# Kernel optimization log

Hardware: AMD Instinct MI355X
Metric: run time of the kernel (lower is better)

## Reference

```python
import jax, jax.numpy as jnp
import numpy as np

B, T, D = 2, 4096, 512
H = 8
HD = D // H  # 64


def setup_inputs() -> dict:
    key = jax.random.key(0)
    k1, k2, k3 = jax.random.split(key, 3)
    x = jax.random.normal(k1, (B, T, D), dtype=jnp.float32)
    w_qkv = jax.random.normal(k2, (3 * D, D), dtype=jnp.float32) * (1.0 / np.sqrt(D))
    w_out = jax.random.normal(k3, (D, D), dtype=jnp.float32) * (1.0 / np.sqrt(D))
    return {"x": x, "w_qkv": w_qkv, "w_out": w_out}


def reference(x, w_qkv, w_out):
    b, t, d = x.shape
    qkv = x @ w_qkv.T                      # [B,T,3D]
    q, k, v = jnp.split(qkv, 3, axis=-1)
    # b t (h d) -> b h t d
    def split_heads(a):
        return a.reshape(b, t, H, HD).transpose(0, 2, 1, 3)
    q, k, v = split_heads(q), split_heads(k), split_heads(v)
    scale = 1.0 / np.sqrt(HD).astype(np.float32)
    scores = jnp.einsum('bhqd,bhkd->bhqk', q, k) * scale  # [B,H,T,T]
    causal = jnp.tril(jnp.ones((t, t), dtype=bool))        # keep lower triangle
    scores = jnp.where(causal[None, None], scores, -jnp.inf)
    attn = jax.nn.softmax(scores, axis=-1)
    out = jnp.einsum('bhqk,bhkd->bhqd', attn, v)           # [B,H,T,HD]
    out = out.transpose(0, 2, 1, 3).reshape(b, t, d)       # b h t d -> b t (h d)
    return out @ w_out.T
```

## Files before the change

### kernel.cpp

```cpp
#include <hip/hip_runtime.h>
#include <hip/hip_bf16.h>

#define BB 2
#define TT 4096
#define DD 512
#define HH 8
#define HD 64
#define M_TOT (BB*TT)
#define N_QKV (3*DD)

typedef __attribute__((ext_vector_type(8))) __bf16 bf16x8;
typedef __attribute__((ext_vector_type(4))) float f32x4;

#define MFMA32(a,b,c) __builtin_amdgcn_mfma_f32_16x16x32_bf16((a),(b),(c),0,0,0)

#define SCALE_L2E 0.18033688011112443f
#define SHIFT_L2E 11.541560327111707f

static __device__ __forceinline__ unsigned short f2bf(float f) {
    union { float f; unsigned u; } v; v.f = f;
    return (unsigned short)((v.u + 0x8000u) >> 16);
}
static __device__ __forceinline__ unsigned short f2bf_t(float f) {
    union { float f; unsigned u; } v; v.f = f;
    return (unsigned short)(v.u >> 16);
}

static __device__ __forceinline__ bf16x8 load8(const unsigned short* p) {
    bf16x8 v;
    __builtin_memcpy(&v, p, 16);
    return v;
}

static __device__ __forceinline__ bf16x8 ones_frag() {
    unsigned short u[8];
    #pragma unroll
    for (int i = 0; i < 8; i++) u[i] = 0x3F80;
    bf16x8 v; __builtin_memcpy(&v, u, 16);
    return v;
}

#define GLDS(gp, lp) __builtin_amdgcn_global_load_lds( \
    (const __attribute__((address_space(1))) unsigned int*)(gp), \
    (__attribute__((address_space(3))) unsigned int*)(lp), 16, 0, 0)

#define NX4 (M_TOT*DD/4)
#define NW4 (N_QKV*DD/4)
#define NO4 (DD*DD/4)
__global__ __launch_bounds__(256) void cast_all(
        const float* __restrict__ x, const float* __restrict__ wqkv,
        const float* __restrict__ wout,
        unsigned short* __restrict__ xb, unsigned short* __restrict__ wqkvb,
        unsigned short* __restrict__ woutb) {
    int i = blockIdx.x * 256 + threadIdx.x;
    const float* s; unsigned short* d; int j;
    if (i < NX4)            { s = x;    d = xb;    j = i; }
    else if (i < NX4 + NW4) { s = wqkv; d = wqkvb; j = i - NX4; }
    else                    { s = wout; d = woutb; j = i - NX4 - NW4; }
    float4 f = ((const float4*)s)[j];
    ushort4 o;
    o.x = f2bf(f.x); o.y = f2bf(f.y); o.z = f2bf(f.z); o.w = f2bf(f.w);
    ((ushort4*)d)[j] = o;
}

__global__ __launch_bounds__(256) void qkv_gemm(
        const unsigned short* __restrict__ xb,
        const unsigned short* __restrict__ wb,
        unsigned short* __restrict__ qb,
        unsigned short* __restrict__ kb,
        unsigned short* __restrict__ vtb) {
    __shared__ union {
        struct { unsigned short As[128 * 32]; unsigned short Bs[128 * 32]; } g;
        unsigned short vt[4][64][72];
    } sm;
    int tid = threadIdx.x;
    int w = tid >> 6, lane = tid & 63;
    int lrow = lane & 15, quad = lane >> 4;
    int bn = blockIdx.x % (N_QKV / 128);
    int bm = blockIdx.x / (N_QKV / 128);
    int m0 = bm * 128, n0 = bn * 128;
    int wm = w >> 1, wn = w & 1;

    f32x4 c[4][4];
    #pragma unroll
    for (int i = 0; i < 4; i++)
        #pragma unroll
        for (int j = 0; j < 4; j++) c[i][j] = (f32x4){0.f, 0.f, 0.f, 0.f};

    for (int k0 = 0; k0 < DD; k0 += 32) {
        #pragma unroll
        for (int j = 0; j < 2; j++) {
            int ch = j * 256 + tid;
            int row = ch >> 2, kc = ch & 3;
            GLDS(xb + (size_t)(m0 + row) * DD + k0 + kc * 8,
                 (char*)sm.g.As + (size_t)(j * 256 + w * 64) * 16);
        }
        #pragma unroll
        for (int j = 0; j < 2; j++) {
            int ch = j * 256 + tid;
            int row = ch >> 2, kc = ch & 3;
            GLDS(wb + (size_t)(n0 + row) * DD + k0 + kc * 8,
                 (char*)sm.g.Bs + (size_t)(j * 256 + w * 64) * 16);
        }
        __syncthreads();
        bf16x8 a[4], b[4];
        #pragma unroll
        for (int mf = 0; mf < 4; mf++) a[mf] = load8(&sm.g.As[(wm * 64 + mf * 16 + lrow) * 32 + quad * 8]);
        #pragma unroll
        for (int nf = 0; nf < 4; nf++) b[nf] = load8(&sm.g.Bs[(wn * 64 + nf * 16 + lrow) * 32 + quad * 8]);
        #pragma unroll
        for (int mf = 0; mf < 4; mf++)
            #pragma unroll
            for (int nf = 0; nf < 4; nf++)
                c[mf][nf] = MFMA32(a[mf], b[nf], c[mf][nf]);
        __syncthreads();
    }

    int m0w = m0 + wm * 64, n0w = n0 + wn * 64;
    int which = n0w >> 9;
    int h = (n0w & 511) >> 6;
    if (which < 2) {
        unsigned short* dst = (which == 0) ? qb : kb;
        #pragma unroll
        for (int mf = 0; mf < 4; mf++) {
            #pragma unroll
            for (int r = 0; r < 4; r++) {
                int m = m0w + mf * 16 + quad * 4 + r;
                int t = m & (TT - 1), bi = m >> 12;
                size_t hb = (size_t)(bi * HH + h) * TT + t;
                #pragma unroll
                for (int nf = 0; nf < 4; nf++)
                    dst[hb * HD + nf * 16 + lrow] = f2bf(c[mf][nf][r]);
            }
        }
    } else {
        #pragma unroll
        for (int mf = 0; mf < 4; mf++)
            #pragma unroll
            for (int r = 0; r < 4; r++)
                #pragma unroll
                for (int nf = 0; nf < 4; nf++)
                    sm.vt[w][nf * 16 + lrow][mf * 16 + quad * 4 + r] = f2bf(c[mf][nf][r]);
        int bi = m0w >> 12, t0 = m0w & (TT - 1);
        size_t hb = (size_t)(bi * HH + h) * HD;
        #pragma unroll
        for (int i = 0; i < 8; i++) {
            int d = i * 8 + (lane >> 3);
            int tc = (lane & 7) * 8;
            bf16x8 v;
            __builtin_memcpy(&v, &sm.vt[w][d][tc], 16);
            __builtin_memcpy(vtb + (hb + d) * TT + t0 + tc, &v, 16);
        }
    }
}

__global__ __launch_bounds__(512) void attn_kernel(
        const unsigned short* __restrict__ qb,
        const unsigned short* __restrict__ kb,
        const unsigned short* __restrict__ vtb,
        unsigned short* __restrict__ attnb) {
    __shared__ union {
        unsigned short p[8][64][68];
        float c[4][64][66];
    } sm;

    const f32x4 ZERO4 = {0.f, 0.f, 0.f, 0.f};
    int w = threadIdx.x >> 6;
    int lane = threadIdx.x & 63;
    int lrow = lane & 15, quad = lane >> 4;
    int bh = blockIdx.x & 15;
    int pr = blockIdx.x >> 4;
    int bi = bh >> 3, h = bh & 7;

    const unsigned short* qh = qb + (size_t)bh * TT * HD;
    const unsigned short* kh = kb + (size_t)bh * TT * HD;
    const unsigned short* vth = vtb + (size_t)bh * HD * TT;
    bf16x8 ones = ones_frag();

    for (int half = 0; half < 2; half++) {
        int qt = half ? (63 - pr) : pr;
        int q0 = qt * 64;

        bf16x8 qf[4][2];
        #pragma unroll
        for (int mf = 0; mf < 4; mf++) {
            const unsigned short* qp = qh + (q0 + mf * 16 + lrow) * HD + quad * 8;
            qf[mf][0] = load8(qp);
            qf[mf][1] = load8(qp + 32);
        }

        f32x4 o[4][4];
        f32x4 l[4];
        #pragma unroll
        for (int i = 0; i < 4; i++) {
            l[i] = ZERO4;
            #pragma unroll
            for (int j = 0; j < 4; j++) o[i][j] = ZERO4;
        }

        for (int kt = w; kt <= qt; kt += 8) {
            int kbase = kt * 64;
            bool diag = (kt == qt);
            bf16x8 kf[4][2], vf[4][2];
            #pragma unroll
            for (int nf = 0; nf < 4; nf++) {
                const unsigned short* kp = kh + (kbase + nf * 16 + lrow) * HD + quad * 8;
                kf[nf][0] = load8(kp);
                kf[nf][1] = load8(kp + 32);
                const unsigned short* vp = vth + (nf * 16 + lrow) * TT + kbase + quad * 8;
                vf[nf][0] = load8(vp);
                vf[nf][1] = load8(vp + 32);
            }
            #pragma unroll
            for (int mf = 0; mf < 4; mf++) {
                #pragma unroll
                for (int nf = 0; nf < 4; nf++) {
                    if (diag && nf > mf) {
                        #pragma unroll
                        for (int r = 0; r < 4; r++)
                            sm.p[w][mf * 16 + quad * 4 + r][nf * 16 + lrow] = 0;
                    } else {
                        f32x4 s = MFMA32(qf[mf][0], kf[nf][0], ZERO4);
                        s = MFMA32(qf[mf][1], kf[nf][1], s);
                        #pragma unroll
                        for (int r = 0; r < 4; r++) {
                            float p = __builtin_amdgcn_exp2f(s[r] * SCALE_L2E - SHIFT_L2E);
                            if (diag && nf == mf && lrow > quad * 4 + r) p = 0.f;
                            sm.p[w][mf * 16 + quad * 4 + r][nf * 16 + lrow] = f2bf_t(p);
                        }
                    }
                }
                bf16x8 pa0, pa1;
                __builtin_memcpy(&pa0, &sm.p[w][mf * 16 + lrow][quad * 8], 16);
                __builtin_memcpy(&pa1, &sm.p[w][mf * 16 + lrow][32 + quad * 8], 16);
                __builtin_amdgcn_s_setprio(1);
                l[mf] = MFMA32(pa0, ones, l[mf]);
                l[mf] = MFMA32(pa1, ones, l[mf]);
                #pragma unroll
                for (int nfd = 0; nfd < 4; nfd++) {
                    o[mf][nfd] = MFMA32(pa0, vf[nfd][0], o[mf][nfd]);
                    o[mf][nfd] = MFMA32(pa1, vf[nfd][1], o[mf][nfd]);
                }
                __builtin_amdgcn_s_setprio(0);
            }
        }

        __syncthreads();
        if (w >= 4) {
            int cb = w - 4;
            #pragma unroll
            for (int mf = 0; mf < 4; mf++)
                #pragma unroll
                for (int r = 0; r < 4; r++) {
                    int row = mf * 16 + quad * 4 + r;
                    #pragma unroll
                    for (int nfd = 0; nfd < 4; nfd++)
                        sm.c[cb][row][nfd * 16 + lrow] = o[mf][nfd][r];
                    if (lrow == 0) sm.c[cb][row][64] = l[mf][r];
                }
        }
        __syncthreads();
        if (w < 4) {
            #pragma unroll
            for (int mf = 0; mf < 4; mf++)
                #pragma unroll
                for (int r = 0; r < 4; r++) {
                    int row = mf * 16 + quad * 4 + r;
                    #pragma unroll
                    for (int nfd = 0; nfd < 4; nfd++)
                        sm.c[w][row][nfd * 16 + lrow] += o[mf][nfd][r];
                    if (lrow == 0) sm.c[w][row][64] += l[mf][r];
                }
        }
        __syncthreads();
        {
            int q = threadIdx.x >> 3, dseg = (threadIdx.x & 7) * 8;
            const float* r0 = &sm.c[0][q][0];
            const float* r1 = &sm.c[1][q][0];
            const float* r2 = &sm.c[2][q][0];
            const float* r3 = &sm.c[3][q][0];
            float inv = 1.0f / (r0[64] + r1[64] + r2[64] + r3[64]);
            unsigned outp[4];
            #pragma unroll
            for (int i = 0; i < 4; i++) {
                int c0 = dseg + 2 * i, c1 = dseg + 2 * i + 1;
                float a0 = (r0[c0] + r1[c0] + r2[c0] + r3[c0]) * inv;
                float a1 = (r0[c1] + r1[c1] + r2[c1] + r3[c1]) * inv;
                outp[i] = (unsigned)f2bf_t(a0) | ((unsigned)f2bf_t(a1) << 16);
            }
            unsigned short* dst = attnb + ((size_t)(bi * TT + q0 + q)) * DD + h * HD + dseg;
            __builtin_memcpy(dst, outp, 16);
        }
        __syncthreads();
    }
}

__global__ __launch_bounds__(256) void proj_gemm(
        const unsigned short* __restrict__ ab,
        const unsigned short* __restrict__ wb,
        float* __restrict__ out) {
    __shared__ unsigned short As[64 * 32];
    __shared__ unsigned short Bs[128 * 32];
    int tid = threadIdx.x;
    int w = tid >> 6, lane = tid & 63;
    int lrow = lane & 15, quad = lane >> 4;
    int bn = blockIdx.x % (DD / 128);
    int bm = blockIdx.x / (DD / 128);
    int m0 = bm * 64, n0 = bn * 128;

    f32x4 c[4][2];
    #pragma unroll
    for (int i = 0; i < 4; i++)
        #pragma unroll
        for (int j = 0; j < 2; j++) c[i][j] = (f32x4){0.f, 0.f, 0.f, 0.f};

    for (int k0 = 0; k0 < DD; k0 += 32) {
        {
            int ch = tid;
            int row = ch >> 2, kc = ch & 3;
            GLDS(ab + (size_t)(m0 + row) * DD + k0 + kc * 8,
                 (char*)As + (size_t)(w * 64) * 16);
        }
        #pragma unroll
        for (int j = 0; j < 2; j++) {
            int ch = j * 256 + tid;
            int row = ch >> 2, kc = ch & 3;
            GLDS(wb + (size_t)(n0 + row) * DD + k0 + kc * 8,
                 (char*)Bs + (size_t)(j * 256 + w * 64) * 16);
        }
        __syncthreads();
        bf16x8 a[4], b[2];
        #pragma unroll
        for (int mf = 0; mf < 4; mf++) a[mf] = load8(&As[(mf * 16 + lrow) * 32 + quad * 8]);
        #pragma unroll
        for (int nf = 0; nf < 2; nf++) b[nf] = load8(&Bs[(w * 32 + nf * 16 + lrow) * 32 + quad * 8]);
        #pragma unroll
        for (int mf = 0; mf < 4; mf++)
            #pragma unroll
            for (int nf = 0; nf < 2; nf++)
                c[mf][nf] = MFMA32(a[mf], b[nf], c[mf][nf]);
        __syncthreads();
    }

    #pragma unroll
    for (int mf = 0; mf < 4; mf++) {
        #pragma unroll
        for (int r = 0; r < 4; r++) {
            int m = m0 + mf * 16 + quad * 4 + r;
            #pragma unroll
            for (int nf = 0; nf < 2; nf++) {
                int n = n0 + w * 32 + nf * 16 + lrow;
                out[(size_t)m * DD + n] = c[mf][nf][r];
            }
        }
    }
}

extern "C" void kernel_launch(void* const* d_in, const int* in_sizes, int n_in,
                              void* d_out, int out_size, void* d_ws, size_t ws_size,
                              hipStream_t stream) {
    const float* x    = (const float*)d_in[0];
    const float* wqkv = (const float*)d_in[1];
    const float* wout = (const float*)d_in[2];
    float* out = (float*)d_out;

    char* ws = (char*)d_ws;
    unsigned short* xb    = (unsigned short*)ws; ws += (size_t)M_TOT * DD * 2;
    unsigned short* wqkvb = (unsigned short*)ws; ws += (size_t)N_QKV * DD * 2;
    unsigned short* woutb = (unsigned short*)ws; ws += (size_t)DD * DD * 2;
    unsigned short* qb    = (unsigned short*)ws; ws += (size_t)BB * HH * TT * HD * 2;
    unsigned short* kb    = (unsigned short*)ws; ws += (size_t)BB * HH * TT * HD * 2;
    unsigned short* vtb   = (unsigned short*)ws; ws += (size_t)BB * HH * HD * TT * 2;
    unsigned short* attnb = (unsigned short*)ws; ws += (size_t)M_TOT * DD * 2;

    cast_all<<<(NX4 + NW4 + NO4) / 256, 256, 0, stream>>>(x, wqkv, wout, xb, wqkvb, woutb);

    qkv_gemm<<<(M_TOT / 128) * (N_QKV / 128), 256, 0, stream>>>(xb, wqkvb, qb, kb, vtb);

    attn_kernel<<<512, 512, 0, stream>>>(qb, kb, vtb, attnb);

    proj_gemm<<<(M_TOT / 64) * (DD / 128), 256, 0, stream>>>(attnb, woutb, out);
}
```

Measured before the change: 192.9 us.

## Split attention waves into two query-row groups with 4-way key partitioning

The 8 waves of each attention block are reorganised into two groups, each owning 32 of the 64 query rows, with 4 waves per group splitting the key tiles instead of all 8 waves sharing full 64-row tiles. This halves per-wave Q, O and softmax-sum register state and shrinks the LDS scratch. V fragments are now loaded in a rolling A/B double-buffer interleaved with the PV MFMAs, and the launch bounds add a minimum-occupancy hint. The cost is that each K/V tile is loaded by both groups, doubling K/V global traffic, and the key split per group is coarser, which may worsen load balance on short causal rows.

```diff
diff --git a/kernel.cpp b/kernel.cpp
--- a/kernel.cpp
+++ b/kernel.cpp
@@ -154,20 +154,22 @@
     }
 }
 
-__global__ __launch_bounds__(512) void attn_kernel(
+__global__ __launch_bounds__(512, 4) void attn_kernel(
         const unsigned short* __restrict__ qb,
         const unsigned short* __restrict__ kb,
         const unsigned short* __restrict__ vtb,
         unsigned short* __restrict__ attnb) {
     __shared__ union {
-        unsigned short p[8][64][68];
-        float c[4][64][66];
+        unsigned short p[8][32][68];
+        float c[2][2][32][66];
     } sm;
 
     const f32x4 ZERO4 = {0.f, 0.f, 0.f, 0.f};
     int w = threadIdx.x >> 6;
     int lane = threadIdx.x & 63;
     int lrow = lane & 15, quad = lane >> 4;
+    int g = w >> 2;
+    int kp = w & 3;
     int bh = blockIdx.x & 15;
     int pr = blockIdx.x >> 4;
     int bi = bh >> 3, h = bh & 7;
@@ -181,41 +183,43 @@
         int qt = half ? (63 - pr) : pr;
         int q0 = qt * 64;
 
-        bf16x8 qf[4][2];
-        #pragma unroll
-        for (int mf = 0; mf < 4; mf++) {
-            const unsigned short* qp = qh + (q0 + mf * 16 + lrow) * HD + quad * 8;
+        bf16x8 qf[2][2];
+        #pragma unroll
+        for (int mf = 0; mf < 2; mf++) {
+            const unsigned short* qp = qh + (q0 + g * 32 + mf * 16 + lrow) * HD + quad * 8;
             qf[mf][0] = load8(qp);
             qf[mf][1] = load8(qp + 32);
         }
 
-        f32x4 o[4][4];
-        f32x4 l[4];
-        #pragma unroll
-        for (int i = 0; i < 4; i++) {
+        f32x4 o[2][4];
+        f32x4 l[2];
+        #pragma unroll
+        for (int i = 0; i < 2; i++) {
             l[i] = ZERO4;
             #pragma unroll
             for (int j = 0; j < 4; j++) o[i][j] = ZERO4;
         }
 
-        for (int kt = w; kt <= qt; kt += 8) {
+        for (int kt = kp; kt <= qt; kt += 4) {
             int kbase = kt * 64;
             bool diag = (kt == qt);
-            bf16x8 kf[4][2], vf[4][2];
+
+            bf16x8 kf[4][2];
             #pragma unroll
             for (int nf = 0; nf < 4; nf++) {
-                const unsigned short* kp = kh + (kbase + nf * 16 + lrow) * HD + quad * 8;
-                kf[nf][0] = load8(kp);
-                kf[nf][1] = load8(kp + 32);
-                const unsigned short* vp = vth + (nf * 16 + lrow) * TT + kbase + quad * 8;
-                vf[nf][0] = load8(vp);
-                vf[nf][1] = load8(vp + 32);
+                const unsigned short* kpp = kh + (kbase + nf * 16 + lrow) * HD + quad * 8;
+                kf[nf][0] = load8(kpp);
+                kf[nf][1] = load8(kpp + 32);
             }
-            #pragma unroll
-            for (int mf = 0; mf < 4; mf++) {
+            const unsigned short* vbase = vth + (size_t)lrow * TT + kbase + quad * 8;
+            bf16x8 vA0 = load8(vbase);
+            bf16x8 vA1 = load8(vbase + 32);
+
+            #pragma unroll
+            for (int mf = 0; mf < 2; mf++) {
                 #pragma unroll
                 for (int nf = 0; nf < 4; nf++) {
-                    if (diag && nf > mf) {
+                    if (diag && nf > mf + 2 * g) {
                         #pragma unroll
                         for (int r = 0; r < 4; r++)
                             sm.p[w][mf * 16 + quad * 4 + r][nf * 16 + lrow] = 0;
@@ -225,67 +229,91 @@
                         #pragma unroll
                         for (int r = 0; r < 4; r++) {
                             float p = __builtin_amdgcn_exp2f(s[r] * SCALE_L2E - SHIFT_L2E);
-                            if (diag && nf == mf && lrow > quad * 4 + r) p = 0.f;
+                            if (diag && nf == mf + 2 * g && lrow > quad * 4 + r) p = 0.f;
                             sm.p[w][mf * 16 + quad * 4 + r][nf * 16 + lrow] = f2bf_t(p);
                         }
                     }
                 }
-                bf16x8 pa0, pa1;
-                __builtin_memcpy(&pa0, &sm.p[w][mf * 16 + lrow][quad * 8], 16);
-                __builtin_memcpy(&pa1, &sm.p[w][mf * 16 + lrow][32 + quad * 8], 16);
-                __builtin_amdgcn_s_setprio(1);
-                l[mf] = MFMA32(pa0, ones, l[mf]);
-                l[mf] = MFMA32(pa1, ones, l[mf]);
-                #pragma unroll
-                for (int nfd = 0; nfd < 4; nfd++) {
-                    o[mf][nfd] = MFMA32(pa0, vf[nfd][0], o[mf][nfd]);
-                    o[mf][nfd] = MFMA32(pa1, vf[nfd][1], o[mf][nfd]);
-                }
-                __builtin_amdgcn_s_setprio(0);
             }
-        }
-
-        __syncthreads();
-        if (w >= 4) {
-            int cb = w - 4;
-            #pragma unroll
-            for (int mf = 0; mf < 4; mf++)
+
+            bf16x8 pa00, pa01, pa10, pa11;
+            __builtin_memcpy(&pa00, &sm.p[w][lrow][quad * 8], 16);
+            __builtin_memcpy(&pa01, &sm.p[w][lrow][32 + quad * 8], 16);
+            __builtin_memcpy(&pa10, &sm.p[w][16 + lrow][quad * 8], 16);
+            __builtin_memcpy(&pa11, &sm.p[w][16 + lrow][32 + quad * 8], 16);
+
+            __builtin_amdgcn_s_setprio(1);
+            l[0] = MFMA32(pa00, ones, l[0]);
+            l[0] = MFMA32(pa01, ones, l[0]);
+            l[1] = MFMA32(pa10, ones, l[1]);
+            l[1] = MFMA32(pa11, ones, l[1]);
+
+            bf16x8 vB0, vB1;
+            vB0 = load8(vbase + 16 * TT);
+            vB1 = load8(vbase + 16 * TT + 32);
+            o[0][0] = MFMA32(pa00, vA0, o[0][0]);
+            o[0][0] = MFMA32(pa01, vA1, o[0][0]);
+            o[1][0] = MFMA32(pa10, vA0, o[1][0]);
+            o[1][0] = MFMA32(pa11, vA1, o[1][0]);
+            vA0 = load8(vbase + 32 * TT);
+            vA1 = load8(vbase + 32 * TT + 32);
+            o[0][1] = MFMA32(pa00, vB0, o[0][1]);
+            o[0][1] = MFMA32(pa01, vB1, o[0][1]);
+            o[1][1] = MFMA32(pa10, vB0, o[1][1]);
+            o[1][1] = MFMA32(pa11, vB1, o[1][1]);
+            vB0 = load8(vbase + 48 * TT);
+            vB1 = load8(vbase + 48 * TT + 32);
+            o[0][2] = MFMA32(pa00, vA0, o[0][2]);
+            o[0][2] = MFMA32(pa01, vA1, o[0][2]);
+            o[1][2] = MFMA32(pa10, vA0, o[1][2]);
+            o[1][2] = MFMA32(pa11, vA1, o[1][2]);
+            o[0][3] = MFMA32(pa00, vB0, o[0][3]);
+            o[0][3] = MFMA32(pa01, vB1, o[0][3]);
+            o[1][3] = MFMA32(pa10, vB0, o[1][3]);
+            o[1][3] = MFMA32(pa11, vB1, o[1][3]);
+            __builtin_amdgcn_s_setprio(0);
+        }
+
+        __syncthreads();
+        if (kp >= 2) {
+            int cb = kp - 2;
+            #pragma unroll
+            for (int mf = 0; mf < 2; mf++)
                 #pragma unroll
                 for (int r = 0; r < 4; r++) {
                     int row = mf * 16 + quad * 4 + r;
                     #pragma unroll
                     for (int nfd = 0; nfd < 4; nfd++)
-                        sm.c[cb][row][nfd * 16 + lrow] = o[mf][nfd][r];
-                    if (lrow == 0) sm.c[cb][row][64] = l[mf][r];
+                        sm.c[g][cb][row][nfd * 16 + lrow] = o[mf][nfd][r];
+                    if (lrow == 0) sm.c[g][cb][row][64] = l[mf][r];
                 }
         }
         __syncthreads();
-        if (w < 4) {
-            #pragma unroll
-            for (int mf = 0; mf < 4; mf++)
+        if (kp < 2) {
+            #pragma unroll
+            for (int mf = 0; mf < 2; mf++)
                 #pragma unroll
                 for (int r = 0; r < 4; r++) {
                     int row = mf * 16 + quad * 4 + r;
                     #pragma unroll
                     for (int nfd = 0; nfd < 4; nfd++)
-                        sm.c[w][row][nfd * 16 + lrow] += o[mf][nfd][r];
-                    if (lrow == 0) sm.c[w][row][64] += l[mf][r];
+                        sm.c[g][kp][row][nfd * 16 + lrow] += o[mf][nfd][r];
+                    if (lrow == 0) sm.c[g][kp][row][64] += l[mf][r];
                 }
         }
         __syncthreads();
         {
             int q = threadIdx.x >> 3, dseg = (threadIdx.x & 7) * 8;
-            const float* r0 = &sm.c[0][q][0];
-            const float* r1 = &sm.c[1][q][0];
-            const float* r2 = &sm.c[2][q][0];
-            const float* r3 = &sm.c[3][q][0];
-            float inv = 1.0f / (r0[64] + r1[64] + r2[64] + r3[64]);
+            int gg = q >> 5, qr = q & 31;
+            const float* r0 = &sm.c[gg][0][qr][0];
+            const float* r1 = &sm.c[gg][1][qr][0];
+            float inv = 1.0f / (r0[64] + r1[64]);
             unsigned outp[4];
             #pragma unroll
             for (int i = 0; i < 4; i++) {
                 int c0 = dseg + 2 * i, c1 = dseg + 2 * i + 1;
-                float a0 = (r0[c0] + r1[c0] + r2[c0] + r3[c0]) * inv;
-                float a1 = (r0[c1] + r1[c1] + r2[c1] + r3[c1]) * inv;
+                float a0 = (r0[c0] + r1[c0]) * inv;
+                float a1 = (r0[c1] + r1[c1]) * inv;
                 outp[i] = (unsigned)f2bf_t(a0) | ((unsigned)f2bf_t(a1) << 16);
             }
             unsigned short* dst = attnb + ((size_t)(bi * TT + q0 + q)) * DD + h * HD + dseg;
```

Result: slower. 227.5 us (+17.9%).
